# Optimization experiments

Measured on AMD Instinct MI355X. Metric: run time of the kernel, lower is better.

## Reference

```python
import jax, jax.numpy as jnp
import numpy as np

B, L, D, C, DEPTH = 2, 1024, 256, 16, 4
N = L // C  # chunks per sequence
EPS = 1.1920929e-07  # torch RMSNorm default eps = finfo(fp32).eps


def rmsnorm(x, w):
    return x * jax.lax.rsqrt(jnp.mean(x * x, axis=-1, keepdims=True) + EPS) * w


def mlp_apply(ws, x):
    # titans MLP: x @ W0, then silu -> @ W1, ... (works for batched [*,d,d] weights too)
    for i, w in enumerate(ws):
        if i:
            x = jax.nn.silu(x)
        x = x @ w
    return x


def setup_inputs() -> dict:
    key = jax.random.key(0)
    ks = jax.random.split(key, 10)
    s = np.float32(1.0 / np.sqrt(D))
    return {
        "seq": jax.random.normal(ks[0], (B, L, D), jnp.float32),
        "w_store_norm": jnp.ones((D,), jnp.float32),
        "w_retrieve_norm": jnp.ones((D,), jnp.float32),
        "w_post_norm": jnp.ones((D,), jnp.float32),
        "Wq": jax.random.normal(ks[1], (D, D), jnp.float32) * s,
        "Wkv": jax.random.normal(ks[2], (D, 2 * D), jnp.float32) * s,
        "w_adapt": jax.random.normal(ks[3], (D,), jnp.float32) * s,
        "w_mom": jax.random.normal(ks[4], (D,), jnp.float32) * s,
        "w_decay": jax.random.normal(ks[5], (D,), jnp.float32) * s,
        "W0": jax.random.normal(ks[6], (D, D), jnp.float32) * s,
        "W1": jax.random.normal(ks[7], (D, D), jnp.float32) * s,
        "W2": jax.random.normal(ks[8], (D, D), jnp.float32) * s,
        "W3": jax.random.normal(ks[9], (D, D), jnp.float32) * s,
    }


def _forward(seq, w_store_norm, w_retrieve_norm, w_post_norm, Wq, Wkv,
             w_adapt, w_mom, w_decay, W0, W1, W2, W3):
    ws = (W0, W1, W2, W3)

    # ---------------- store_memories ----------------
    sn = rmsnorm(seq, w_store_norm)                      # [B,L,D]; L already multiple of C
    cm = sn.reshape(B, N, C, D).mean(axis=2)             # per-chunk mean [B,N,D]
    adaptive_lr = jax.nn.sigmoid(cm @ w_adapt)           # [B,N]
    adaptive_mom = jax.nn.sigmoid(cm @ w_mom)[..., None]   # [B,N,1]
    decay = jax.nn.sigmoid(cm @ w_decay)[..., None]        # [B,N,1]

    kv = sn @ Wkv                                        # [B,L,2D]
    keys = kv[..., :D].reshape(B * N, C, D)
    vals = kv[..., D:].reshape(B * N, C, D)

    def chunk_loss(params, k, v):
        pred = mlp_apply(params, k)                      # [C,D]
        return jnp.sum(jnp.mean((pred - v) ** 2, axis=-1))

    # per-chunk grads wrt the 4 MLP weights (past weights are zero at init)
    grads = jax.vmap(jax.grad(chunk_loss), in_axes=(None, 0, 0))(ws, keys, vals)
    g = jnp.stack(grads, axis=1).reshape(B, N, DEPTH * D * D)  # packed 'b n *'
    surprise = -adaptive_lr[..., None] * g               # [B,N,P]

    def op(l, r):
        al, xl = l
        ar, xr = r
        return (al * ar, xl * ar + xr)                   # x_t = a_t*x_{t-1} + b_t

    _, momentum = jax.lax.associative_scan(op, (adaptive_mom, surprise), axis=1)
    _, updates = jax.lax.associative_scan(op, (1.0 - decay, momentum), axis=1)
    upd = updates.reshape(B, N, DEPTH, D, D)

    # per-chunk fast weights: base params + cumulative update
    fast_ws = tuple((w + upd[:, :, i]).reshape(B * N, D, D) for i, w in enumerate(ws))

    # ---------------- retrieve_memories ----------------
    rn = rmsnorm(seq, w_retrieve_norm)[:, C - 1:]        # [B, L-C+1, D]
    rn = jnp.pad(rn, ((0, 0), (0, C - 1), (0, 0)))       # pad back up to [B,L,D]
    q = (rn @ Wq).reshape(B * N, C, D)
    out = mlp_apply(fast_ws, q).reshape(B, L, D)         # batched fast-weight MLP
    out = rmsnorm(out, w_post_norm)
    out = jnp.pad(out, ((0, 0), (C - 1, 0), (0, 0)))[:, :-(C - 1)]  # shift by C-1
    return out


def reference(seq, w_store_norm, w_retrieve_norm, w_post_norm, Wq, Wkv,
              w_adapt, w_mom, w_decay, W0, W1, W2, W3):
    return _forward(seq, w_store_norm, w_retrieve_norm, w_post_norm, Wq, Wkv,
                    w_adapt, w_mom, w_decay, W0, W1, W2, W3)
```

## Files before the change

### kernel.cpp

```cpp
#include <hip/hip_runtime.h>
#include <hip/hip_bf16.h>

typedef __attribute__((ext_vector_type(8)))  short s8v;
typedef __attribute__((ext_vector_type(4)))  float f4v;
typedef _Float16 h4 __attribute__((ext_vector_type(4)));
typedef __attribute__((ext_vector_type(4))) unsigned short u4v;

constexpr int NCn  = 128;
constexpr int DDn  = 65536;
constexpr int XP   = 264;
constexpr float EPSf = 1.1920929e-07f;

__device__ __forceinline__ float sigm(float x){ return 1.0f/(1.0f + expf(-x)); }
__device__ __forceinline__ float silu_(float x){ return x * sigm(x); }
__device__ __forceinline__ float dsilu_(float x){ float s = sigm(x); return s*(1.0f + x*(1.0f - s)); }

__device__ __forceinline__ unsigned short f2b(float x){
    __hip_bfloat16 b = __float2bfloat16(x);
    unsigned short u; __builtin_memcpy(&u, &b, 2); return u;
}
__device__ __forceinline__ float b2f(unsigned short u){
    __hip_bfloat16 b; __builtin_memcpy(&b, &u, 2); return __bfloat162float(b);
}
__device__ __forceinline__ h4 ldh4(const unsigned short* p){
    h4 r; __builtin_memcpy(&r, p, 8); return r;
}

__device__ __forceinline__ int fidx(int row, int col){
    return (((row >> 4)*8 + (col >> 5))*4 + ((col >> 3) & 3))*128 + (row & 15)*8 + (col & 7);
}

__global__ __launch_bounds__(256) void ktw(const float* __restrict__ Wq,
        const float* __restrict__ Wkv, const float* __restrict__ W0,
        const float* __restrict__ W1, const float* __restrict__ W2,
        const float* __restrict__ W3, unsigned short* __restrict__ WTb,
        unsigned short* __restrict__ WqTb, unsigned short* __restrict__ WkvTb,
        unsigned short* __restrict__ Wb){
    int z = blockIdx.z;
    if (z >= 6){
        const float* S = (z==6)?W1:(z==7)?W2:W3;
        size_t idx = (((size_t)blockIdx.y*8 + blockIdx.x)*256 + threadIdx.x)*2;
        float2 v = *(const float2*)(S + idx);
        ushort2 u; u.x = f2b(v.x); u.y = f2b(v.y);
        int row = (int)(idx >> 8), col = (int)(idx & 255);
        *(ushort2*)(Wb + (size_t)(z-6)*DDn + fidx(row, col)) = u;
        return;
    }
    __shared__ float tl[32][33];
    if (z != 5 && blockIdx.y >= 8) return;
    const float* S; unsigned short* T; int C;
    if (z < 4){ S = (z==0)?W0:(z==1)?W1:(z==2)?W2:W3; T = WTb + (size_t)z*DDn; C = 256; }
    else if (z == 4){ S = Wq; T = WqTb; C = 256; }
    else { S = Wkv; T = WkvTb; C = 512; }
    int k0 = blockIdx.x*32, j0 = blockIdx.y*32;
    int tx = threadIdx.x & 31, ty = threadIdx.x >> 5;
    #pragma unroll
    for (int p = 0; p < 4; ++p)
        tl[ty + 8*p][tx] = S[(size_t)(k0 + ty + 8*p)*C + j0 + tx];
    __syncthreads();
    #pragma unroll
    for (int p = 0; p < 4; ++p){
        int r = j0 + ty + 8*p, k = k0 + tx;
        T[fidx(r, k)] = f2b(tl[tx][ty + 8*p]);
    }
}

__global__ __launch_bounds__(1024, 1) void kfb(const float* __restrict__ seq,
        const float* __restrict__ wsn,
        const unsigned short* __restrict__ WkvTb, const unsigned short* __restrict__ WTb,
        const unsigned short* __restrict__ Wb,
        const float* __restrict__ wa, const float* __restrict__ wm,
        const float* __restrict__ wdk,
        float* __restrict__ momg, float* __restrict__ decg,
        unsigned short* __restrict__ XT, unsigned short* __restrict__ GT){
    __shared__ unsigned short xs[16][XP];
    __shared__ unsigned short xl[4][16][XP];
    __shared__ unsigned short Gs[16][XP];
    __shared__ float red3[16][4];
    int tid = threadIdx.x, w = tid >> 6, lane = tid & 63;
    int m16 = lane & 15, q16 = lane >> 4;
    int g = blockIdx.x;
    int n0 = w*16;
    size_t fb = (size_t)w*4096 + q16*128 + m16*8;

    {
        const float4 xv = *(const float4*)(seq + ((size_t)g*16 + w)*256 + lane*4);
        const float4 wv = *(const float4*)(wsn + lane*4);
        float ssq = xv.x*xv.x + xv.y*xv.y + xv.z*xv.z + xv.w*xv.w;
        #pragma unroll
        for (int off = 32; off; off >>= 1) ssq += __shfl_xor(ssq, off, 64);
        float s2 = rsqrtf(ssq*(1.f/256.f) + EPSf);
        u4v sv;
        sv[0] = f2b(xv.x*s2*wv.x); sv[1] = f2b(xv.y*s2*wv.y);
        sv[2] = f2b(xv.z*s2*wv.z); sv[3] = f2b(xv.w*s2*wv.w);
        *(u4v*)(&xs[w][lane*4]) = sv;
    }
    __syncthreads();

    float sc;
    {
        int d2 = tid & 255, qt = tid >> 8;
        float a = 0.f;
        #pragma unroll
        for (int c = 0; c < 4; ++c)
            a += b2f(xs[qt*4 + c][d2]);
        float cm = a * (1.f/16.f);
        float s0 = cm*wa[d2], s1 = cm*wm[d2], s2 = cm*wdk[d2];
        #pragma unroll
        for (int off = 32; off; off >>= 1){
            s0 += __shfl_down(s0, off, 64);
            s1 += __shfl_down(s1, off, 64);
            s2 += __shfl_down(s2, off, 64);
        }
        if (lane == 0){ red3[w][0] = s0; red3[w][1] = s1; red3[w][2] = s2; }
        __syncthreads();
        float da = 0.f, dm = 0.f, dc = 0.f;
        #pragma unroll
        for (int i = 0; i < 16; ++i){
            da += red3[i][0]; dm += red3[i][1]; dc += red3[i][2];
        }
        sc = -2.f * sigm(da) * (1.f/256.f);
        if (tid == 0){ momg[g] = sigm(dm); decg[g] = sigm(dc); }
    }

    s8v af[8];
    #pragma unroll
    for (int i = 0; i < 8; ++i) af[i] = *(const s8v*)(&xs[m16][q16*8 + i*32]);

    s8v bpre[8];
    #pragma unroll
    for (int i = 0; i < 8; ++i) bpre[i] = *(const s8v*)(WTb + fb + i*512);

    f4v vacc;
    {
        f4v ka = {0.f,0.f,0.f,0.f}, va = {0.f,0.f,0.f,0.f};
        const unsigned short* brK = WkvTb + fb;
        const unsigned short* brV = WkvTb + (size_t)DDn + fb;
        #pragma unroll
        for (int i = 0; i < 8; ++i){
            s8v bK = *(const s8v*)(brK + i*512);
            s8v bV = *(const s8v*)(brV + i*512);
            ka = __builtin_amdgcn_mfma_f32_16x16x32_bf16(af[i], bK, ka, 0, 0, 0);
            va = __builtin_amdgcn_mfma_f32_16x16x32_bf16(af[i], bV, va, 0, 0, 0);
        }
        vacc = va;
        #pragma unroll
        for (int r = 0; r < 4; ++r) xl[0][4*q16 + r][n0 + m16] = f2b(ka[r]);
    }

    f4v hreg[3];
    #pragma unroll
    for (int l = 0; l < 3; ++l){
        __syncthreads();
        s8v xa[8];
        #pragma unroll
        for (int i = 0; i < 8; ++i)
            xa[i] = *(const s8v*)(&xl[l][m16][q16*8 + i*32]);
        s8v bcur[8];
        #pragma unroll
        for (int i = 0; i < 8; ++i) bcur[i] = bpre[i];
        const unsigned short* nxt = WTb + (size_t)(l+1)*DDn + fb;
        #pragma unroll
        for (int i = 0; i < 8; ++i) bpre[i] = *(const s8v*)(nxt + i*512);
        f4v acc = {0.f,0.f,0.f,0.f};
        #pragma unroll
        for (int i = 0; i < 8; ++i)
            acc = __builtin_amdgcn_mfma_f32_16x16x32_bf16(xa[i], bcur[i], acc, 0, 0, 0);
        hreg[l] = acc;
        #pragma unroll
        for (int r = 0; r < 4; ++r)
            xl[l+1][4*q16 + r][n0 + m16] = f2b(silu_(acc[r]));
    }
    __syncthreads();

    {
        int d = tid & 255, qt = tid >> 8;
        #pragma unroll
        for (int l = 0; l < 4; ++l){
            h4 v;
            #pragma unroll
            for (int j = 0; j < 4; ++j)
                v[j] = (_Float16)b2f(xl[l][qt*4 + j][d]);
            *(h4*)(XT + (((size_t)l*128 + g)*256 + d)*16 + qt*4) = v;
        }
    }

    {
        s8v xa[8];
        #pragma unroll
        for (int i = 0; i < 8; ++i)
            xa[i] = *(const s8v*)(&xl[3][m16][q16*8 + i*32]);
        s8v bcur[8];
        #pragma unroll
        for (int i = 0; i < 8; ++i) bcur[i] = bpre[i];
        const unsigned short* nxt = Wb + (size_t)2*DDn + fb;
        #pragma unroll
        for (int i = 0; i < 8; ++i) bpre[i] = *(const s8v*)(nxt + i*512);
        f4v acc = {0.f,0.f,0.f,0.f};
        #pragma unroll
        for (int i = 0; i < 8; ++i)
            acc = __builtin_amdgcn_mfma_f32_16x16x32_bf16(xa[i], bcur[i], acc, 0, 0, 0);
        #pragma unroll
        for (int r = 0; r < 4; ++r)
            Gs[4*q16 + r][n0 + m16] = f2b(sc * (acc[r] - vacc[r]));
    }
    __syncthreads();
    {
        int d = tid & 255, qt = tid >> 8;
        h4 v;
        #pragma unroll
        for (int j = 0; j < 4; ++j)
            v[j] = (_Float16)b2f(Gs[qt*4 + j][d]);
        *(h4*)(GT + (((size_t)3*128 + g)*256 + d)*16 + qt*4) = v;
    }

    #pragma unroll
    for (int l = 3; l >= 1; --l){
        s8v gfa[8];
        #pragma unroll
        for (int i = 0; i < 8; ++i)
            gfa[i] = *(const s8v*)(&Gs[m16][q16*8 + i*32]);
        s8v bcur[8];
        #pragma unroll
        for (int i = 0; i < 8; ++i) bcur[i] = bpre[i];
        if (l > 1){
            const unsigned short* nxt = Wb + (size_t)(l-2)*DDn + fb;
            #pragma unroll
            for (int i = 0; i < 8; ++i) bpre[i] = *(const s8v*)(nxt + i*512);
        }
        f4v acc = {0.f,0.f,0.f,0.f};
        #pragma unroll
        for (int i = 0; i < 8; ++i)
            acc = __builtin_amdgcn_mfma_f32_16x16x32_bf16(gfa[i], bcur[i], acc, 0, 0, 0);
        f4v gn;
        #pragma unroll
        for (int r = 0; r < 4; ++r)
            gn[r] = acc[r] * dsilu_(hreg[l-1][r]);
        __syncthreads();
        #pragma unroll
        for (int r = 0; r < 4; ++r)
            Gs[4*q16 + r][n0 + m16] = f2b(gn[r]);
        __syncthreads();
        {
            int d = tid & 255, qt = tid >> 8;
            h4 v;
            #pragma unroll
            for (int j = 0; j < 4; ++j)
                v[j] = (_Float16)b2f(Gs[qt*4 + j][d]);
            *(h4*)(GT + (((size_t)(l-1)*128 + g)*256 + d)*16 + qt*4) = v;
        }
    }
}

__global__ __launch_bounds__(64, 1) void kck(const unsigned short* __restrict__ XT,
        const unsigned short* __restrict__ GT, const float* __restrict__ momg,
        const float* __restrict__ decg, unsigned short* __restrict__ ucpb){
    int lane = threadIdx.x;
    int m16 = lane & 15, q16 = lane >> 4;
    int rt = blockIdx.x, ct = blockIdx.y, bl = blockIdx.z;
    int b = bl >> 2, l = bl & 3;
    int dr = rt*16 + m16;
    int dc = ct*16 + m16;
    const unsigned short* Gb  = GT + ((size_t)l*128 + b*64)*4096 + (size_t)dr*16 + q16*4;
    const unsigned short* Xb2 = XT + ((size_t)l*128 + b*64)*4096 + (size_t)dc*16 + q16*4;
    int col = ct*16 + m16;
    int fo0 = ((rt*8 + (col >> 5))*4 + ((col >> 3) & 3))*128 + (4*q16)*8 + (col & 7);
    f4v us = {0.f,0.f,0.f,0.f}, ms = {0.f,0.f,0.f,0.f};
    #pragma unroll 4
    for (int n = 0; n < 64; ++n){
        float mo = momg[b*64 + n], de = 1.f - decg[b*64 + n];
        h4 a  = ldh4(Gb  + (size_t)n*4096);
        h4 xb = ldh4(Xb2 + (size_t)n*4096);
        f4v z = {0.f,0.f,0.f,0.f};
        f4v s = __builtin_amdgcn_mfma_f32_16x16x16f16(a, xb, z, 0, 0, 0);
        size_t cb = ((size_t)bl*64 + n)*65536;
        #pragma unroll
        for (int r = 0; r < 4; ++r){
            float mn = mo*ms[r] + s[r];
            float un = de*us[r] + mn;
            ms[r] = mn; us[r] = un;
            ucpb[cb + fo0 + r*8] = f2b(un);
        }
    }
}

__global__ __launch_bounds__(1024, 1) void kretr(const float* __restrict__ seq,
        const float* __restrict__ wrn,
        const unsigned short* __restrict__ WqTb, const unsigned short* __restrict__ WTb,
        const unsigned short* __restrict__ ucpb, const float* __restrict__ wpost,
        float* __restrict__ out){
    __shared__ unsigned short xc[2][16][XP];
    __shared__ float red[16][16];
    __shared__ float rs[16];
    int tid = threadIdx.x, w = tid >> 6, lane = tid & 63;
    int m16 = lane & 15, q16 = lane >> 4;
    int g = blockIdx.x;
    int b = g >> 6, nl = g & 63;
    int n0 = w*16;
    size_t fb = (size_t)w*4096 + q16*128 + m16*8;

    {
        int p = nl*16 + w + 15;
        u4v sv = {0,0,0,0};
        if (p < 1024){
            const float4 xv = *(const float4*)(seq + ((size_t)b*1024 + p)*256 + lane*4);
            const float4 wv = *(const float4*)(wrn + lane*4);
            float ssq = xv.x*xv.x + xv.y*xv.y + xv.z*xv.z + xv.w*xv.w;
            #pragma unroll
            for (int off = 32; off; off >>= 1) ssq += __shfl_xor(ssq, off, 64);
            float s2 = rsqrtf(ssq*(1.f/256.f) + EPSf);
            sv[0] = f2b(xv.x*s2*wv.x); sv[1] = f2b(xv.y*s2*wv.y);
            sv[2] = f2b(xv.z*s2*wv.z); sv[3] = f2b(xv.w*s2*wv.w);
        }
        *(u4v*)(&xc[1][w][lane*4]) = sv;
    }
    __syncthreads();

    {
        s8v a[8];
        #pragma unroll
        for (int i = 0; i < 8; ++i) a[i] = *(const s8v*)(&xc[1][m16][q16*8 + i*32]);
        f4v acc = {0.f,0.f,0.f,0.f};
        const unsigned short* br = WqTb + fb;
        #pragma unroll
        for (int i = 0; i < 8; ++i){
            s8v bb = *(const s8v*)(br + i*512);
            acc = __builtin_amdgcn_mfma_f32_16x16x32_bf16(a[i], bb, acc, 0, 0, 0);
        }
        #pragma unroll
        for (int r = 0; r < 4; ++r) xc[0][4*q16 + r][n0 + m16] = f2b(acc[r]);
    }
    __syncthreads();

    f4v hacc;
    for (int l = 0; l < 4; ++l){
        s8v xa[8];
        #pragma unroll
        for (int i = 0; i < 8; ++i)
            xa[i] = *(const s8v*)(&xc[l & 1][m16][q16*8 + i*32]);
        const unsigned short* br = WTb + (size_t)l*DDn + fb;
        const unsigned short* bu = ucpb + ((size_t)(b*4 + l)*64 + nl)*65536 + fb;
        f4v aW = {0.f,0.f,0.f,0.f}, aU = {0.f,0.f,0.f,0.f};
        #pragma unroll
        for (int i = 0; i < 8; ++i){
            s8v w0 = *(const s8v*)(br + i*512);
            s8v u0 = *(const s8v*)(bu + i*512);
            aW = __builtin_amdgcn_mfma_f32_16x16x32_bf16(xa[i], w0, aW, 0, 0, 0);
            aU = __builtin_amdgcn_mfma_f32_16x16x32_bf16(xa[i], u0, aU, 0, 0, 0);
        }
        #pragma unroll
        for (int r = 0; r < 4; ++r) hacc[r] = aW[r] + aU[r];
        if (l < 3){
            #pragma unroll
            for (int r = 0; r < 4; ++r)
                xc[(l + 1) & 1][4*q16 + r][n0 + m16] = f2b(silu_(hacc[r]));
            __syncthreads();
        }
    }

    float part[4];
    #pragma unroll
    for (int r = 0; r < 4; ++r) part[r] = hacc[r]*hacc[r];
    #pragma unroll
    for (int off = 1; off < 16; off <<= 1)
        #pragma unroll
        for (int r = 0; r < 4; ++r) part[r] += __shfl_xor(part[r], off, 64);
    if (m16 == 0)
        #pragma unroll
        for (int r = 0; r < 4; ++r) red[w][4*q16 + r] = part[r];
    __syncthreads();
    if (tid < 16){
        float s = 0.f;
        #pragma unroll
        for (int i = 0; i < 16; ++i) s += red[i][tid];
        rs[tid] = rsqrtf(s*(1.f/256.f) + EPSf);
    }
    __syncthreads();
    {
        int d = n0 + m16;
        float wp = wpost[d];
        #pragma unroll
        for (int r = 0; r < 4; ++r){
            int c = 4*q16 + r;
            int tp = nl*16 + c + 15;
            if (tp < 1024)
                out[((size_t)b*1024 + tp)*256 + d] = hacc[r]*rs[c]*wp;
        }
    }
    if (nl == 0){
        for (int idx = tid; idx < 15*256; idx += 1024)
            out[(size_t)b*262144 + idx] = 0.f;
    }
}

extern "C" void kernel_launch(void* const* d_in, const int* in_sizes, int n_in,
                              void* d_out, int out_size, void* d_ws, size_t ws_size,
                              hipStream_t stream) {
    const float* seq     = (const float*)d_in[0];
    const float* w_store = (const float*)d_in[1];
    const float* w_retr  = (const float*)d_in[2];
    const float* w_post  = (const float*)d_in[3];
    const float* Wq      = (const float*)d_in[4];
    const float* Wkv     = (const float*)d_in[5];
    const float* w_adapt = (const float*)d_in[6];
    const float* w_mom   = (const float*)d_in[7];
    const float* w_decay = (const float*)d_in[8];
    const float* W0      = (const float*)d_in[9];
    const float* W1      = (const float*)d_in[10];
    const float* W2      = (const float*)d_in[11];
    const float* W3      = (const float*)d_in[12];

    float* momg  = (float*)d_ws;
    float* decg  = momg + NCn;
    unsigned short* WTb   = (unsigned short*)(decg + NCn + 32);
    unsigned short* Wb    = WTb   + 4*(size_t)DDn;
    unsigned short* WqTb  = Wb    + 3*(size_t)DDn;
    unsigned short* WkvTb = WqTb  + (size_t)DDn;
    unsigned short* XT    = WkvTb + 2*(size_t)DDn;
    unsigned short* GT    = XT    + (size_t)4*NCn*4096;
    unsigned short* ucpb  = GT    + (size_t)4*NCn*4096;

    ktw   <<<dim3(8, 16, 9),  256,  0, stream>>>(Wq, Wkv, W0, W1, W2, W3,
                                                 WTb, WqTb, WkvTb, Wb);
    kfb   <<<dim3(NCn),       1024, 0, stream>>>(seq, w_store, WkvTb, WTb, Wb,
                                                 w_adapt, w_mom, w_decay,
                                                 momg, decg, XT, GT);
    kck   <<<dim3(16, 16, 8), 64,   0, stream>>>(XT, GT, momg, decg, ucpb);
    kretr <<<dim3(NCn),       1024, 0, stream>>>(seq, w_retr, WqTb, WTb, ucpb,
                                                 w_post, (float*)d_out);
}
```

Measured before the change: 143.3 us.

## Vectorize kck update stores via LDS transpose and prefetch ucpb in kretr

The cumulative-update kernel now computes two 16-column tiles per block and stages results through a small shared-memory transpose, so each lane writes 4 contiguous bf16 values instead of scattered 2-byte stores. Grid y is halved to match. The retrieval kernel software-prefetches the next layer's fast-weight update fragment into registers while computing the current layer, hiding global load latency. The costs are higher register pressure and an LDS round trip. There is also no barrier between the shared-memory writes and reads in the single-wave block, which relies on wavefront lockstep execution.

```diff
diff --git a/kernel.cpp b/kernel.cpp
--- a/kernel.cpp
+++ b/kernel.cpp
@@ -255,32 +255,52 @@
 __global__ __launch_bounds__(64, 1) void kck(const unsigned short* __restrict__ XT,
         const unsigned short* __restrict__ GT, const float* __restrict__ momg,
         const float* __restrict__ decg, unsigned short* __restrict__ ucpb){
+    __shared__ unsigned short ts[2][16][18];
     int lane = threadIdx.x;
     int m16 = lane & 15, q16 = lane >> 4;
-    int rt = blockIdx.x, ct = blockIdx.y, bl = blockIdx.z;
+    int rt = blockIdx.x, ct0 = blockIdx.y*2, bl = blockIdx.z;
     int b = bl >> 2, l = bl & 3;
     int dr = rt*16 + m16;
-    int dc = ct*16 + m16;
-    const unsigned short* Gb  = GT + ((size_t)l*128 + b*64)*4096 + (size_t)dr*16 + q16*4;
-    const unsigned short* Xb2 = XT + ((size_t)l*128 + b*64)*4096 + (size_t)dc*16 + q16*4;
-    int col = ct*16 + m16;
-    int fo0 = ((rt*8 + (col >> 5))*4 + ((col >> 3) & 3))*128 + (4*q16)*8 + (col & 7);
-    f4v us = {0.f,0.f,0.f,0.f}, ms = {0.f,0.f,0.f,0.f};
+    const unsigned short* Gb = GT + ((size_t)l*128 + b*64)*4096 + (size_t)dr*16 + q16*4;
+    const unsigned short* X0 = XT + ((size_t)l*128 + b*64)*4096
+                             + (size_t)(ct0*16 + m16)*16 + q16*4;
+    const unsigned short* X1 = X0 + 256;
+    int rr = lane & 15, cg = lane >> 4;
+    int off0, off1;
+    {
+        int c0 = ct0*16 + cg*4, c1 = c0 + 16;
+        off0 = ((rt*8 + (c0 >> 5))*4 + ((c0 >> 3) & 3))*128 + rr*8 + (c0 & 7);
+        off1 = ((rt*8 + (c1 >> 5))*4 + ((c1 >> 3) & 3))*128 + rr*8 + (c1 & 7);
+    }
+    f4v us0 = {0.f,0.f,0.f,0.f}, ms0 = {0.f,0.f,0.f,0.f};
+    f4v us1 = {0.f,0.f,0.f,0.f}, ms1 = {0.f,0.f,0.f,0.f};
     #pragma unroll 4
     for (int n = 0; n < 64; ++n){
         float mo = momg[b*64 + n], de = 1.f - decg[b*64 + n];
-        h4 a  = ldh4(Gb  + (size_t)n*4096);
-        h4 xb = ldh4(Xb2 + (size_t)n*4096);
+        h4 a  = ldh4(Gb + (size_t)n*4096);
+        h4 x0 = ldh4(X0 + (size_t)n*4096);
+        h4 x1 = ldh4(X1 + (size_t)n*4096);
         f4v z = {0.f,0.f,0.f,0.f};
-        f4v s = __builtin_amdgcn_mfma_f32_16x16x16f16(a, xb, z, 0, 0, 0);
+        f4v s0 = __builtin_amdgcn_mfma_f32_16x16x16f16(a, x0, z, 0, 0, 0);
+        f4v s1 = __builtin_amdgcn_mfma_f32_16x16x16f16(a, x1, z, 0, 0, 0);
+        #pragma unroll
+        for (int r = 0; r < 4; ++r){
+            float mn0 = mo*ms0[r] + s0[r], un0 = de*us0[r] + mn0;
+            ms0[r] = mn0; us0[r] = un0;
+            ts[0][4*q16 + r][m16] = f2b(un0);
+            float mn1 = mo*ms1[r] + s1[r], un1 = de*us1[r] + mn1;
+            ms1[r] = mn1; us1[r] = un1;
+            ts[1][4*q16 + r][m16] = f2b(un1);
+        }
         size_t cb = ((size_t)bl*64 + n)*65536;
-        #pragma unroll
-        for (int r = 0; r < 4; ++r){
-            float mn = mo*ms[r] + s[r];
-            float un = de*us[r] + mn;
-            ms[r] = mn; us[r] = un;
-            ucpb[cb + fo0 + r*8] = f2b(un);
-        }
+        u4v v0, v1;
+        #pragma unroll
+        for (int j = 0; j < 4; ++j){
+            v0[j] = ts[0][rr][cg*4 + j];
+            v1[j] = ts[1][rr][cg*4 + j];
+        }
+        *(u4v*)(ucpb + cb + off0) = v0;
+        *(u4v*)(ucpb + cb + off1) = v1;
     }
 }
 
@@ -298,6 +318,11 @@
     int b = g >> 6, nl = g & 63;
     int n0 = w*16;
     size_t fb = (size_t)w*4096 + q16*128 + m16*8;
+    const unsigned short* ubase = ucpb + ((size_t)(b*4)*64 + nl)*65536 + fb;
+
+    s8v upre[8];
+    #pragma unroll
+    for (int i = 0; i < 8; ++i) upre[i] = *(const s8v*)(ubase + i*512);
 
     {
         int p = nl*16 + w + 15;
@@ -338,15 +363,21 @@
         #pragma unroll
         for (int i = 0; i < 8; ++i)
             xa[i] = *(const s8v*)(&xc[l & 1][m16][q16*8 + i*32]);
+        s8v ucur[8];
+        #pragma unroll
+        for (int i = 0; i < 8; ++i) ucur[i] = upre[i];
+        if (l < 3){
+            const unsigned short* un = ubase + (size_t)(l+1)*64*65536;
+            #pragma unroll
+            for (int i = 0; i < 8; ++i) upre[i] = *(const s8v*)(un + i*512);
+        }
         const unsigned short* br = WTb + (size_t)l*DDn + fb;
-        const unsigned short* bu = ucpb + ((size_t)(b*4 + l)*64 + nl)*65536 + fb;
         f4v aW = {0.f,0.f,0.f,0.f}, aU = {0.f,0.f,0.f,0.f};
         #pragma unroll
         for (int i = 0; i < 8; ++i){
             s8v w0 = *(const s8v*)(br + i*512);
-            s8v u0 = *(const s8v*)(bu + i*512);
             aW = __builtin_amdgcn_mfma_f32_16x16x32_bf16(xa[i], w0, aW, 0, 0, 0);
-            aU = __builtin_amdgcn_mfma_f32_16x16x32_bf16(xa[i], u0, aU, 0, 0, 0);
+            aU = __builtin_amdgcn_mfma_f32_16x16x32_bf16(xa[i], ucur[i], aU, 0, 0, 0);
         }
         #pragma unroll
         for (int r = 0; r < 4; ++r) hacc[r] = aW[r] + aU[r];
@@ -425,7 +456,7 @@
     kfb   <<<dim3(NCn),       1024, 0, stream>>>(seq, w_store, WkvTb, WTb, Wb,
                                                  w_adapt, w_mom, w_decay,
                                                  momg, decg, XT, GT);
-    kck   <<<dim3(16, 16, 8), 64,   0, stream>>>(XT, GT, momg, decg, ucpb);
+    kck   <<<dim3(16, 8, 8),  64,   0, stream>>>(XT, GT, momg, decg, ucpb);
     kretr <<<dim3(NCn),       1024, 0, stream>>>(seq, w_retr, WqTb, WTb, ucpb,
                                                  w_post, (float*)d_out);
 }
```

Result: no change. 143.7 us (+0.3%).
